# Kernel optimization log

Hardware: AMD Instinct MI355X
Metric: run time of the kernel (lower is better)

## Reference

```python
import jax, jax.numpy as jnp
import numpy as np

EPS = 1e-7  # K.epsilon()
ROUTINGS = 3
NUM_CAPSULE = 32
DIM_CAPSULE = 64

def _squash(x, axis=-1):
    # NOTE: this repo's 'squash' is just L2-ish normalization: x / sqrt(||x||^2 + eps)
    s2 = jnp.sum(jnp.square(x), axis=axis, keepdims=True)
    return x / jnp.sqrt(s2 + EPS)

def setup_inputs() -> dict:
    key = jax.random.key(0)
    k1, k2 = jax.random.split(key)
    u_vecs = jax.random.normal(k1, (32, 1024, 256), dtype=jnp.float32)
    # shared-weight capsule kernel: (1, input_dim_capsule, num_capsule*dim_capsule)
    W = jax.random.normal(k2, (1, 256, NUM_CAPSULE * DIM_CAPSULE), dtype=jnp.float32) * 0.05
    return {"u_vecs": u_vecs, "W": W}

def reference(u_vecs, W):
    B, N, D = u_vecs.shape
    # conv1d with width-1 kernel == matmul over feature dim
    u_hat = jnp.einsum('bnd,dm->bnm', u_vecs, W[0])          # [B, N, NC*DC]
    u_hat = u_hat.reshape(B, N, NUM_CAPSULE, DIM_CAPSULE)
    u_hat = jnp.transpose(u_hat, (0, 2, 1, 3))               # [B, NC, N, DC]

    b = jnp.zeros((B, NUM_CAPSULE, N), dtype=u_hat.dtype)    # routing logits
    v = None
    for i in range(ROUTINGS):
        c = jax.nn.softmax(b, axis=-1)                       # over input capsules
        s = jnp.einsum('bij,bijd->bid', c, u_hat)            # weighted sum
        v = _squash(s)                                       # [B, NC, DC]
        if i < ROUTINGS - 1:
            b = b + jnp.einsum('bid,bijd->bij', v, u_hat)    # agreement update
    return v
```

## Files before the change

### kernel.cpp

```cpp
#include <hip/hip_runtime.h>
#include <math.h>


typedef short v8s __attribute__((ext_vector_type(8)));
typedef short v4s __attribute__((ext_vector_type(4)));
typedef float v4f __attribute__((ext_vector_type(4)));

__device__ __forceinline__ unsigned short f2bf(float x) {
    unsigned u = __float_as_uint(x);
    u = u + 0x7fffu + ((u >> 16) & 1u);
    return (unsigned short)(u >> 16);
}
__device__ __forceinline__ float bf2f(unsigned short h) {
    return __uint_as_float(((unsigned)h) << 16);
}

__global__ __launch_bounds__(256) void k_init(const float* __restrict__ U,
                                              const float* __restrict__ W,
                                              float* __restrict__ t0p,
                                              float* __restrict__ WT) {
    int bid = blockIdx.x, tid = threadIdx.x;
    if (bid < 512) {
        int b = bid >> 4, q = bid & 15;
        const float* Up = U + (((b << 10) + (q << 6)) << 8) + tid;
        float acc = 0.f;
        #pragma unroll 16
        for (int jl = 0; jl < 64; ++jl) acc += Up[jl << 8];
        t0p[(b << 12) + (q << 8) + tid] = acc * (1.0f / 1024.0f);
    } else {
        __shared__ float tile[64 * 65];
        int tix = bid - 512;
        int k0 = (tix >> 5) << 6, c0 = (tix & 31) << 6;
        int cc = tid & 63, g4 = tid >> 6;
        #pragma unroll
        for (int r = 0; r < 16; ++r) {
            int kk = (g4 << 4) + r;
            tile[kk * 65 + cc] = W[(k0 + kk) * 2048 + c0 + cc];
        }
        __syncthreads();
        int kk = tid & 63;
        #pragma unroll
        for (int r = 0; r < 16; ++r) {
            int c = (g4 << 4) + r;
            WT[(c0 + c) * 256 + k0 + kk] = tile[kk * 65 + c];
        }
    }
}

__global__ __launch_bounds__(256) void k_sv(const float* __restrict__ t0p,
                                            const float* __restrict__ tpart,
                                            const float* __restrict__ sefpart,
                                            const float* __restrict__ W,
                                            const float* __restrict__ WT,
                                            short* __restrict__ wbt_h,
                                            short* __restrict__ wbt_l,
                                            float* __restrict__ out,
                                            int mode, int writeOut) {
    __shared__ float t_lds[256];
    __shared__ float spart[256];
    __shared__ __align__(16) float v_lds[64];
    __shared__ __align__(16) v4f spartw[256];
    __shared__ float sefv_s;
    int bid = blockIdx.x, tid = threadIdx.x;
    int b = bid >> 5, iG = bid & 31;
    int bg = (b << 1) | (iG >> 4), il = iG & 15;

    float acc = 0.f;
    if (mode == 0) {
        const float* tb = t0p + (b << 12) + tid;
        #pragma unroll
        for (int q = 0; q < 16; ++q) acc += tb[q << 8];
        if (tid == 0) sefv_s = 1.0f;
    } else {
        const float* tb = tpart + (((bg << 4) + il) << 8) + tid;
        #pragma unroll
        for (int p = 0; p < 16; ++p) acc += tb[p << 18];
        if (tid == 0) {
            float s = 0.f;
            #pragma unroll
            for (int p = 0; p < 16; ++p) s += sefpart[(p << 10) + (bg << 4) + il];
            sefv_s = s;
        }
    }
    t_lds[tid] = acc;
    __syncthreads();

    int d = tid & 63, kq = tid >> 6;
    const float* Wc = W + ((kq << 6) * 2048) + (iG << 6) + d;
    float s = 0.f;
    #pragma unroll 4
    for (int kk = 0; kk < 64; ++kk)
        s += t_lds[(kq << 6) + kk] * Wc[kk * 2048];
    spart[tid] = s;
    __syncthreads();

    if (tid < 64) {
        float sv = spart[tid] + spart[tid + 64] + spart[tid + 128] + spart[tid + 192];
        float n2 = sv * sv;
        #pragma unroll
        for (int m = 1; m < 64; m <<= 1) n2 += __shfl_xor(n2, m, 64);
        float sf = sefv_s;
        float v = sv * rsqrtf(n2 + 1e-7f * sf * sf);
        v_lds[tid] = v;
        if (writeOut) out[(bid << 6) + tid] = v;
    }
    __syncthreads();
    if (writeOut) return;

    int k4 = tid & 63, dq = tid >> 6;
    const float4* WT4 = (const float4*)WT;
    v4f wp = {0.f, 0.f, 0.f, 0.f};
    #pragma unroll
    for (int dd = 0; dd < 16; ++dd) {
        float vv = v_lds[(dq << 4) + dd];
        float4 wt = WT4[((iG << 6) + (dq << 4) + dd) * 64 + k4];
        wp.x += vv * wt.x; wp.y += vv * wt.y; wp.z += vv * wt.z; wp.w += vv * wt.w;
    }
    spartw[(dq << 6) + k4] = wp;
    __syncthreads();
    if (tid < 64) {
        v4f w = spartw[tid] + spartw[64 + tid] + spartw[128 + tid] + spartw[192 + tid];
        float wv4[4] = {w.x, w.y, w.z, w.w};
        unsigned short wh[4], wl[4];
        #pragma unroll
        for (int e = 0; e < 4; ++e) {
            wh[e] = f2bf(wv4[e]);
            wl[e] = f2bf(wv4[e] - bf2f(wh[e]));
        }
        int base = (((bg << 4) + il) << 8) + (tid << 2);
        *(v4s*)&wbt_h[base] = (v4s){(short)wh[0], (short)wh[1], (short)wh[2], (short)wh[3]};
        *(v4s*)&wbt_l[base] = (v4s){(short)wl[0], (short)wl[1], (short)wl[2], (short)wl[3]};
    }
}

__global__ __launch_bounds__(1024, 8) void k_pass(const float* __restrict__ U,
                                                  const short* __restrict__ wbt_h,
                                                  const short* __restrict__ wbt_l,
                                                  float* __restrict__ bmatg,
                                                  float* __restrict__ tpart_out,
                                                  float* __restrict__ sefpart_out,
                                                  int addold) {
    __shared__ short s_U[64 * 268];
    __shared__ short s_wh[16 * 264];
    __shared__ short s_wl[16 * 264];
    __shared__ short s_eh[16 * 72];
    __shared__ short s_el[16 * 72];
    __shared__ float s_red[16 * 320];
    __shared__ float s_sefp[16 * 16];

    const int tid = threadIdx.x, wv = tid >> 6, lane = tid & 63;
    const int quad = lane >> 4, nn = lane & 15;
    const int blk = blockIdx.x;
    const int b = blk & 31, pg = blk >> 5;
    const int p = pg >> 1, g2 = pg & 1;
    const int bg = (b << 1) | g2;
    const int rowbase = (b << 10) + (p << 6);
    const float4* U4 = (const float4*)U;

    const int mt2 = wv & 3, jq = wv >> 2;
    const int rr = (jq << 2) + quad;
    const int jloc = (mt2 << 4) + rr;
    const int ga = (((bg << 10) + (p << 6) + jloc) << 4) + nn;
    float bold = 0.f;
    if (addold) bold = bmatg[ga];

    if (tid < 512) {
        int row = tid >> 5, seg = tid & 31;
        int gidx = (((bg << 4) + row) << 8) + (seg << 3);
        *(v8s*)&s_wh[row * 264 + (seg << 3)] = *(const v8s*)(wbt_h + gidx);
        *(v8s*)&s_wl[row * 264 + (seg << 3)] = *(const v8s*)(wbt_l + gidx);
    }
    {
        int col = tid & 63, row0 = tid >> 6;
        float4 g[4];
        #pragma unroll
        for (int q = 0; q < 4; ++q)
            g[q] = U4[(rowbase + row0 + (q << 4)) * 64 + col];
        #pragma unroll
        for (int q = 0; q < 4; ++q)
            *(v4s*)&s_U[(row0 + (q << 4)) * 268 + (col << 2)] =
                (v4s){(short)f2bf(g[q].x), (short)f2bf(g[q].y),
                      (short)f2bf(g[q].z), (short)f2bf(g[q].w)};
    }
    __syncthreads();

    {
        const int mt = wv & 3, kq = wv >> 2;
        v4f dacc = {0.f, 0.f, 0.f, 0.f};
        #pragma unroll
        for (int c = 0; c < 2; ++c) {
            int kb = (kq << 6) + (c << 5) + (quad << 3);
            v8s a  = *(const v8s*)&s_U[((mt << 4) + nn) * 268 + kb];
            v8s bh = *(const v8s*)&s_wh[nn * 264 + kb];
            v8s bl = *(const v8s*)&s_wl[nn * 264 + kb];
            dacc = __builtin_amdgcn_mfma_f32_16x16x32_bf16(a, bh, dacc, 0, 0, 0);
            dacc = __builtin_amdgcn_mfma_f32_16x16x32_bf16(a, bl, dacc, 0, 0, 0);
        }
        #pragma unroll
        for (int r = 0; r < 4; ++r)
            s_red[wv * 320 + ((quad << 2) + r) * 20 + nn] = dacc[r];
    }
    __syncthreads();

    {
        float val = bold;
        #pragma unroll
        for (int kq = 0; kq < 4; ++kq)
            val += s_red[((kq << 2) + mt2) * 320 + rr * 20 + nn];
        if (!addold) bmatg[ga] = val;
        float e = __expf(val);
        unsigned short eh = f2bf(e);
        s_eh[nn * 72 + jloc] = (short)eh;
        s_el[nn * 72 + jloc] = (short)f2bf(e - bf2f(eh));
        float se = e;
        se += __shfl_xor(se, 16, 64);
        se += __shfl_xor(se, 32, 64);
        if (lane < 16) s_sefp[(wv << 4) + lane] = se;
    }
    __syncthreads();

    {
        v4f tacc = {0.f, 0.f, 0.f, 0.f};
        const int k0 = wv << 4;
        #pragma unroll
        for (int jc = 0; jc < 2; ++jc) {
            v8s aeh = *(const v8s*)&s_eh[nn * 72 + (jc << 5) + (quad << 3)];
            v8s ael = *(const v8s*)&s_el[nn * 72 + (jc << 5) + (quad << 3)];
            short bu[8];
            #pragma unroll
            for (int jj = 0; jj < 8; ++jj)
                bu[jj] = s_U[((jc << 5) + (quad << 3) + jj) * 268 + k0 + nn];
            v8s bf = (v8s){bu[0], bu[1], bu[2], bu[3], bu[4], bu[5], bu[6], bu[7]};
            tacc = __builtin_amdgcn_mfma_f32_16x16x32_bf16(aeh, bf, tacc, 0, 0, 0);
            tacc = __builtin_amdgcn_mfma_f32_16x16x32_bf16(ael, bf, tacc, 0, 0, 0);
        }
        #pragma unroll
        for (int r = 0; r < 4; ++r) {
            int i = (quad << 2) + r;
            tpart_out[(((((p << 6) + bg) << 4) + i) << 8) + k0 + nn] = tacc[r];
        }
    }
    if (tid < 16) {
        float ss = 0.f;
        #pragma unroll
        for (int w = 0; w < 16; ++w) ss += s_sefp[(w << 4) + tid];
        sefpart_out[(p << 10) + (bg << 4) + tid] = ss;
    }
}

extern "C" void kernel_launch(void* const* d_in, const int* in_sizes, int n_in,
                              void* d_out, int out_size, void* d_ws, size_t ws_size,
                              hipStream_t stream) {
    const float* U = (const float*)d_in[0];
    const float* W = (const float*)d_in[1];
    float* out = (float*)d_out;
    float* ws = (float*)d_ws;

    float* t0p   = ws;
    float* WT    = t0p + 131072;
    float* bmatg = WT + 524288;
    float* tp    = bmatg + 1048576;
    float* sef   = tp + 4194304;
    short* wbt_h = (short*)(sef + 16384);
    short* wbt_l = wbt_h + 262144;

    k_init<<<640, 256, 0, stream>>>(U, W, t0p, WT);
    k_sv<<<1024, 256, 0, stream>>>(t0p, nullptr, nullptr, W, WT,
                                   wbt_h, wbt_l, out, 0, 0);
    k_pass<<<1024, 1024, 0, stream>>>(U, wbt_h, wbt_l, bmatg, tp, sef, 0);
    k_sv<<<1024, 256, 0, stream>>>(t0p, tp, sef, W, WT,
                                   wbt_h, wbt_l, out, 1, 0);
    k_pass<<<1024, 1024, 0, stream>>>(U, wbt_h, wbt_l, bmatg, tp, sef, 1);
    k_sv<<<1024, 256, 0, stream>>>(t0p, tp, sef, W, WT,
                                   wbt_h, wbt_l, out, 1, 1);
}
```

Measured before the change: 131.4 us.

## Pre-convert U to swizzled bf16, DMA into LDS, fold logits into weight sums

The init kernel now writes a bf16 copy of U with a rotated (XOR-free, add-based) column swizzle, so each pass kernel loads half the bytes straight into LDS through global_load_lds instead of converting fp32 in registers. Routing logits are no longer stored in and reloaded from a global bmatg buffer. Instead the projected v·W vectors are summed across iterations in a new wsum buffer, which is linear algebra since b accumulates v·u_hat. LDS row padding is replaced by the rotation swizzle to avoid bank conflicts. The cost is an extra full pass over U in init to write the bf16 copy.

```diff
diff --git a/kernel.cpp b/kernel.cpp
--- a/kernel.cpp
+++ b/kernel.cpp
@@ -14,14 +14,38 @@
 __device__ __forceinline__ float bf2f(unsigned short h) {
     return __uint_as_float(((unsigned)h) << 16);
 }
+__device__ __forceinline__ void dma16(const void* g, void* l) {
+    __builtin_amdgcn_global_load_lds(
+        (const __attribute__((address_space(1))) unsigned int*)g,
+        (__attribute__((address_space(3))) unsigned int*)l, 16, 0, 0);
+}
 
 __global__ __launch_bounds__(256) void k_init(const float* __restrict__ U,
                                               const float* __restrict__ W,
                                               float* __restrict__ t0p,
-                                              float* __restrict__ WT) {
+                                              float* __restrict__ WT,
+                                              short* __restrict__ Ubf16) {
     int bid = blockIdx.x, tid = threadIdx.x;
     if (bid < 512) {
         int b = bid >> 4, q = bid & 15;
+        const float4* U4 = (const float4*)U;
+        #pragma unroll
+        for (int it = 0; it < 8; ++it) {
+            int idx = (it << 8) + tid;
+            int jl = idx >> 5, ch = idx & 31;
+            int j = (q << 6) + jl;
+            float4 g0 = U4[(((b << 10) + j) << 6) + (ch << 1)];
+            float4 g1 = U4[(((b << 10) + j) << 6) + (ch << 1) + 1];
+            int rot = ((ch << 3) + ((j & 15) << 3)) & 255;
+            *(v8s*)&Ubf16[((size_t)((b << 10) + j) << 8) + rot] =
+                (v8s){(short)f2bf(g0.x), (short)f2bf(g0.y),
+                      (short)f2bf(g0.z), (short)f2bf(g0.w),
+                      (short)f2bf(g1.x), (short)f2bf(g1.y),
+                      (short)f2bf(g1.z), (short)f2bf(g1.w)};
+        }
+    } else if (bid < 1024) {
+        int b2 = bid - 512;
+        int b = b2 >> 4, q = b2 & 15;
         const float* Up = U + (((b << 10) + (q << 6)) << 8) + tid;
         float acc = 0.f;
         #pragma unroll 16
@@ -29,7 +53,7 @@
         t0p[(b << 12) + (q << 8) + tid] = acc * (1.0f / 1024.0f);
     } else {
         __shared__ float tile[64 * 65];
-        int tix = bid - 512;
+        int tix = bid - 1024;
         int k0 = (tix >> 5) << 6, c0 = (tix & 31) << 6;
         int cc = tid & 63, g4 = tid >> 6;
         #pragma unroll
@@ -52,6 +76,7 @@
                                             const float* __restrict__ sefpart,
                                             const float* __restrict__ W,
                                             const float* __restrict__ WT,
+                                            float* __restrict__ wsum,
                                             short* __restrict__ wbt_h,
                                             short* __restrict__ wbt_l,
                                             float* __restrict__ out,
@@ -121,28 +146,34 @@
     if (tid < 64) {
         v4f w = spartw[tid] + spartw[64 + tid] + spartw[128 + tid] + spartw[192 + tid];
         float wv4[4] = {w.x, w.y, w.z, w.w};
+        int wsidx = (((bg << 4) + il) << 8) + (tid << 2);
+        if (mode != 0) {
+            float4 old = *(const float4*)&wsum[wsidx];
+            wv4[0] += old.x; wv4[1] += old.y; wv4[2] += old.z; wv4[3] += old.w;
+        }
+        *(float4*)&wsum[wsidx] =
+            make_float4(wv4[0], wv4[1], wv4[2], wv4[3]);
         unsigned short wh[4], wl[4];
         #pragma unroll
         for (int e = 0; e < 4; ++e) {
             wh[e] = f2bf(wv4[e]);
             wl[e] = f2bf(wv4[e] - bf2f(wh[e]));
         }
-        int base = (((bg << 4) + il) << 8) + (tid << 2);
+        int rotk = ((tid << 2) + (il << 3)) & 255;
+        int base = (((bg << 4) + il) << 8) + rotk;
         *(v4s*)&wbt_h[base] = (v4s){(short)wh[0], (short)wh[1], (short)wh[2], (short)wh[3]};
         *(v4s*)&wbt_l[base] = (v4s){(short)wl[0], (short)wl[1], (short)wl[2], (short)wl[3]};
     }
 }
 
-__global__ __launch_bounds__(1024, 8) void k_pass(const float* __restrict__ U,
+__global__ __launch_bounds__(1024, 8) void k_pass(const short* __restrict__ Ubf16,
                                                   const short* __restrict__ wbt_h,
                                                   const short* __restrict__ wbt_l,
-                                                  float* __restrict__ bmatg,
                                                   float* __restrict__ tpart_out,
-                                                  float* __restrict__ sefpart_out,
-                                                  int addold) {
-    __shared__ short s_U[64 * 268];
-    __shared__ short s_wh[16 * 264];
-    __shared__ short s_wl[16 * 264];
+                                                  float* __restrict__ sefpart_out) {
+    __shared__ short s_U[64 * 256];
+    __shared__ short s_wh[16 * 256];
+    __shared__ short s_wl[16 * 256];
     __shared__ short s_eh[16 * 72];
     __shared__ short s_el[16 * 72];
     __shared__ float s_red[16 * 320];
@@ -155,32 +186,18 @@
     const int p = pg >> 1, g2 = pg & 1;
     const int bg = (b << 1) | g2;
     const int rowbase = (b << 10) + (p << 6);
-    const float4* U4 = (const float4*)U;
-
-    const int mt2 = wv & 3, jq = wv >> 2;
-    const int rr = (jq << 2) + quad;
-    const int jloc = (mt2 << 4) + rr;
-    const int ga = (((bg << 10) + (p << 6) + jloc) << 4) + nn;
-    float bold = 0.f;
-    if (addold) bold = bmatg[ga];
-
-    if (tid < 512) {
-        int row = tid >> 5, seg = tid & 31;
-        int gidx = (((bg << 4) + row) << 8) + (seg << 3);
-        *(v8s*)&s_wh[row * 264 + (seg << 3)] = *(const v8s*)(wbt_h + gidx);
-        *(v8s*)&s_wl[row * 264 + (seg << 3)] = *(const v8s*)(wbt_l + gidx);
-    }
+
     {
-        int col = tid & 63, row0 = tid >> 6;
-        float4 g[4];
-        #pragma unroll
-        for (int q = 0; q < 4; ++q)
-            g[q] = U4[(rowbase + row0 + (q << 4)) * 64 + col];
-        #pragma unroll
-        for (int q = 0; q < 4; ++q)
-            *(v4s*)&s_U[(row0 + (q << 4)) * 268 + (col << 2)] =
-                (v4s){(short)f2bf(g[q].x), (short)f2bf(g[q].y),
-                      (short)f2bf(g[q].z), (short)f2bf(g[q].w)};
+        const char* ug = (const char*)Ubf16 + ((size_t)rowbase << 9);
+        dma16(ug + (wv << 11) + (lane << 4), (char*)s_U + (wv << 11));
+        dma16(ug + (wv << 11) + 1024 + (lane << 4), (char*)s_U + (wv << 11) + 1024);
+        if (wv < 8) {
+            const char* wg = (const char*)wbt_h + (bg << 13) + (wv << 10);
+            dma16(wg + (lane << 4), (char*)s_wh + (wv << 10));
+        } else {
+            const char* wg = (const char*)wbt_l + (bg << 13) + ((wv - 8) << 10);
+            dma16(wg + (lane << 4), (char*)s_wl + ((wv - 8) << 10));
+        }
     }
     __syncthreads();
 
@@ -190,9 +207,10 @@
         #pragma unroll
         for (int c = 0; c < 2; ++c) {
             int kb = (kq << 6) + (c << 5) + (quad << 3);
-            v8s a  = *(const v8s*)&s_U[((mt << 4) + nn) * 268 + kb];
-            v8s bh = *(const v8s*)&s_wh[nn * 264 + kb];
-            v8s bl = *(const v8s*)&s_wl[nn * 264 + kb];
+            int rk = (kb + (nn << 3)) & 255;
+            v8s a  = *(const v8s*)&s_U[(((mt << 4) + nn) << 8) + rk];
+            v8s bh = *(const v8s*)&s_wh[(nn << 8) + rk];
+            v8s bl = *(const v8s*)&s_wl[(nn << 8) + rk];
             dacc = __builtin_amdgcn_mfma_f32_16x16x32_bf16(a, bh, dacc, 0, 0, 0);
             dacc = __builtin_amdgcn_mfma_f32_16x16x32_bf16(a, bl, dacc, 0, 0, 0);
         }
@@ -203,11 +221,13 @@
     __syncthreads();
 
     {
-        float val = bold;
+        const int mt2 = wv & 3, jq = wv >> 2;
+        const int rr = (jq << 2) + quad;
+        const int jloc = (mt2 << 4) + rr;
+        float val = 0.f;
         #pragma unroll
         for (int kq = 0; kq < 4; ++kq)
             val += s_red[((kq << 2) + mt2) * 320 + rr * 20 + nn];
-        if (!addold) bmatg[ga] = val;
         float e = __expf(val);
         unsigned short eh = f2bf(e);
         s_eh[nn * 72 + jloc] = (short)eh;
@@ -228,8 +248,11 @@
             v8s ael = *(const v8s*)&s_el[nn * 72 + (jc << 5) + (quad << 3)];
             short bu[8];
             #pragma unroll
-            for (int jj = 0; jj < 8; ++jj)
-                bu[jj] = s_U[((jc << 5) + (quad << 3) + jj) * 268 + k0 + nn];
+            for (int jj = 0; jj < 8; ++jj) {
+                int jrow = (jc << 5) + (quad << 3) + jj;
+                int rk = (k0 + nn + ((jrow & 15) << 3)) & 255;
+                bu[jj] = s_U[(jrow << 8) + rk];
+            }
             v8s bf = (v8s){bu[0], bu[1], bu[2], bu[3], bu[4], bu[5], bu[6], bu[7]};
             tacc = __builtin_amdgcn_mfma_f32_16x16x32_bf16(aeh, bf, tacc, 0, 0, 0);
             tacc = __builtin_amdgcn_mfma_f32_16x16x32_bf16(ael, bf, tacc, 0, 0, 0);
@@ -258,19 +281,20 @@
 
     float* t0p   = ws;
     float* WT    = t0p + 131072;
-    float* bmatg = WT + 524288;
-    float* tp    = bmatg + 1048576;
+    float* wsum  = WT + 524288;
+    float* tp    = wsum + 262144;
     float* sef   = tp + 4194304;
     short* wbt_h = (short*)(sef + 16384);
     short* wbt_l = wbt_h + 262144;
-
-    k_init<<<640, 256, 0, stream>>>(U, W, t0p, WT);
-    k_sv<<<1024, 256, 0, stream>>>(t0p, nullptr, nullptr, W, WT,
+    short* Ubf16 = wbt_l + 262144;
+
+    k_init<<<1152, 256, 0, stream>>>(U, W, t0p, WT, Ubf16);
+    k_sv<<<1024, 256, 0, stream>>>(t0p, nullptr, nullptr, W, WT, wsum,
                                    wbt_h, wbt_l, out, 0, 0);
-    k_pass<<<1024, 1024, 0, stream>>>(U, wbt_h, wbt_l, bmatg, tp, sef, 0);
-    k_sv<<<1024, 256, 0, stream>>>(t0p, tp, sef, W, WT,
+    k_pass<<<1024, 1024, 0, stream>>>(Ubf16, wbt_h, wbt_l, tp, sef);
+    k_sv<<<1024, 256, 0, stream>>>(t0p, tp, sef, W, WT, wsum,
                                    wbt_h, wbt_l, out, 1, 0);
-    k_pass<<<1024, 1024, 0, stream>>>(U, wbt_h, wbt_l, bmatg, tp, sef, 1);
-    k_sv<<<1024, 256, 0, stream>>>(t0p, tp, sef, W, WT,
+    k_pass<<<1024, 1024, 0, stream>>>(Ubf16, wbt_h, wbt_l, tp, sef);
+    k_sv<<<1024, 256, 0, stream>>>(t0p, tp, sef, W, WT, wsum,
                                    wbt_h, wbt_l, out, 1, 1);
 }
```

Result: slower. 140.7 us (+7.0%).
